# Kernel optimization log

Hardware: AMD Instinct MI355X
Metric: run time of the kernel (lower is better)

Reference implementation:

```python
import jax, jax.numpy as jnp
import numpy as np

BS, HW, HIDDEN, TOK, NTOK = 32, 1024, 256, 768, 2048


def setup_inputs() -> dict:
    key = jax.random.key(0)
    ks = jax.random.split(key, 6)
    s = 0.02  # init scale for weights
    return {
        "src": jax.random.normal(ks[0], (HW, BS, HIDDEN), jnp.float32),
        "codebook": jax.random.normal(ks[1], (NTOK, TOK), jnp.float32),
        "w_head": jax.random.normal(ks[2], (TOK, HIDDEN), jnp.float32) * s,
        "w_tail": jax.random.normal(ks[3], (HIDDEN, TOK), jnp.float32) * s,
        "w_pos": jax.random.normal(ks[4], (TOK, TOK), jnp.float32) * s,
        "b_pos": jnp.zeros((TOK,), jnp.float32),
        "w_gate": jax.random.normal(ks[5], (2, 2 * TOK), jnp.float32) * s,
        "h": 32,
        "w": 32,
    }


def reference(src, codebook, w_head, w_tail, w_pos, b_pos, w_gate, h, w):
    N, bs, hidden = src.shape  # [num_visu_token, bs, hidden_dim]
    tok = codebook.shape[1]
    # permute(1,2,0).view(bs,-1,h,w)
    x = jnp.transpose(src, (1, 2, 0)).reshape(bs, hidden, h, w)
    # conv_head: 1x1 conv, no bias
    xq = jnp.einsum("bchw,oc->bohw", x, w_head)  # [bs, tok, h, w]
    # raw-memory reshape, matches torch .view(-1, token_dim)
    flat = xq.reshape(-1, tok)  # [bs*h*w, tok]
    d = (
        jnp.sum(flat * flat, axis=1, keepdims=True)
        - 2.0 * flat @ codebook.T
        + jnp.sum(codebook * codebook, axis=1)[None, :]
    )
    indices = jnp.argmin(d, axis=1)  # [bs*h*w]
    quantized = codebook[indices]  # gather
    # straight-through estimator
    quantized = flat + jax.lax.stop_gradient(quantized - flat)
    # pos_align linear
    quantized = quantized @ w_pos.T + b_pos
    # view(bs, N, tok).permute(0,2,1).view(bs,-1,h,w)
    emb = jnp.transpose(quantized.reshape(bs, N, tok), (0, 2, 1)).reshape(bs, tok, h, w)
    # gated fusion
    gate_in = jnp.concatenate([emb, xq], axis=1)  # [bs, 2*tok, h, w]
    scores = jax.nn.softmax(jnp.einsum("bchw,oc->bohw", gate_in, w_gate), axis=1)
    fused = emb * scores[:, 0:1] + xq * scores[:, 1:2]
    # conv_tail 1x1, then flatten(2).permute(2,0,1)
    out = jnp.einsum("bchw,oc->bohw", fused, w_tail)  # [bs, hidden, h, w]
    out = jnp.transpose(out.reshape(bs, hidden, -1), (2, 0, 1))  # [h*w, bs, hidden]
    return out, indices
```

## Files before the change

kernel.cpp:

```cpp
#include <hip/hip_runtime.h>
#include <cstdint>

#define BSZ 32
#define NVIS 1024
#define HID 256
#define TOKD 768
#define NCODE 2048
#define NPIX 32768

typedef unsigned short u16;
typedef _Float16 half8 __attribute__((ext_vector_type(8)));
typedef unsigned short ushort8 __attribute__((ext_vector_type(8)));
typedef unsigned short u16x4 __attribute__((ext_vector_type(4)));
using f32x4 = __attribute__((ext_vector_type(4))) float;

#define AS1 __attribute__((address_space(1)))
#define AS3 __attribute__((address_space(3)))

__device__ __forceinline__ f32x4 mfmaF16(half8 a, half8 b, f32x4 c) {
  return __builtin_amdgcn_mfma_f32_16x16x32_f16(a, b, c, 0, 0, 0);
}

__device__ __forceinline__ unsigned long long pack_key(float d, int idx) {
  unsigned int b = __float_as_uint(d);
  b = (b & 0x80000000u) ? ~b : (b | 0x80000000u);
  return ((unsigned long long)b << 32) | (unsigned int)idx;
}

__device__ __forceinline__ void split16(float v, u16& h, u16& l) {
  union { _Float16 f; u16 u; } a, b;
  a.f = (_Float16)v;
  float hf = (float)a.f;
  b.f = (_Float16)(v - hf);
  h = a.u; l = b.u;
}

__global__ __launch_bounds__(256)
void prep1(const float* __restrict__ cb, const float* __restrict__ wh,
           const float* __restrict__ wt, const float* __restrict__ wp,
           const float* __restrict__ wg, const float* __restrict__ bp,
           u16* __restrict__ cbh, u16* __restrict__ cbl,
           u16* __restrict__ whh, u16* __restrict__ whl,
           float* __restrict__ cbn, float* __restrict__ Mm, float* __restrict__ uv,
           float* __restrict__ Gt, float* __restrict__ g2,
           float* __restrict__ ct0, float* __restrict__ cg) {
  const int bid = blockIdx.x, tid = threadIdx.x;
  if (bid < 6144) {
    int i = bid*256 + tid;
    u16 h, l; split16(cb[i], h, l);
    cbh[i] = h; cbl[i] = l;
  } else if (bid < 6912) {
    int i = (bid - 6144)*256 + tid;
    u16 h, l; split16(wh[i], h, l);
    whh[i] = h; whl[i] = l;
  } else if (bid < 7424) {
    int n = (bid - 6912)*4 + (tid >> 6);
    int lane = tid & 63;
    float a = 0.f;
#pragma unroll
    for (int i = 0; i < 12; ++i) { float v = cb[(long)n*TOKD + lane + 64*i]; a += v*v; }
#pragma unroll
    for (int off = 32; off; off >>= 1) a += __shfl_down(a, off);
    if (lane == 0) cbn[n] = a;
  } else if (bid < 7680) {
    int c2 = bid - 7424, c1 = tid;
    float acc = 0.f;
    for (int t = 0; t < TOKD; ++t) acc += wh[t*HID + c1] * wt[(long)c2*TOKD + t];
    Mm[c1*HID + c2] = acc;
  } else if (bid < 7682) {
    int o = bid - 7680, c1 = tid;
    float acc = 0.f;
    for (int t = 0; t < TOKD; ++t) acc += wh[t*HID + c1] * wg[o*(2*TOKD) + TOKD + t];
    uv[o*HID + c1] = acc;
  } else if (bid < 8450) {
    int rbid = bid - 7682;
    int c = rbid & 255, part = rbid >> 8;
    int tp = part*256 + tid;
    float acc = 0.f;
    for (int t = 0; t < TOKD; ++t) acc += wt[(long)c*TOKD + t] * wp[(long)t*TOKD + tp];
    Gt[(long)tp*HID + c] = acc;
  } else if (bid < 8453) {
    int tp = (bid - 8450)*256 + tid;
    float a0 = 0.f, a1 = 0.f;
    for (int t = 0; t < TOKD; ++t) {
      float wv = wp[(long)t*TOKD + tp];
      a0 += wv * wg[t];
      a1 += wv * wg[2*TOKD + t];
    }
    g2[tp] = a0; g2[TOKD + tp] = a1;
  } else if (bid < 8454) {
    int c = tid;
    float a = 0.f;
    for (int t = 0; t < TOKD; ++t) a += bp[t] * wt[(long)c*TOKD + t];
    ct0[c] = a;
  } else {
    int o = tid >> 6, lane = tid & 63;
    if (o < 2) {
      float a = 0.f;
      for (int t = lane; t < TOKD; t += 64) a += bp[t] * wg[o*(2*TOKD) + t];
#pragma unroll
      for (int off = 32; off; off >>= 1) a += __shfl_down(a, off);
      if (lane == 0) cg[o] = a;
    }
  }
}

__global__ __launch_bounds__(256)
void prep2(const float* __restrict__ cb, const float* __restrict__ Gt,
           const float* __restrict__ ct0, const float* __restrict__ g2,
           const float* __restrict__ cg, float* __restrict__ tc,
           float* __restrict__ gA) {
  __shared__ float cbs[8][TOKD];
  const int n0 = blockIdx.x * 8, tid = threadIdx.x;
  for (int i = tid; i < 8*TOKD; i += 256) cbs[i / TOKD][i % TOKD] = cb[(long)n0*TOKD + i];
  __syncthreads();
  float acc[8] = {};
  for (int t = 0; t < TOKD; ++t) {
    float gv = Gt[(long)t*HID + tid];
#pragma unroll
    for (int i = 0; i < 8; ++i) acc[i] += cbs[i][t] * gv;
  }
  float c0v = ct0[tid];
#pragma unroll
  for (int i = 0; i < 8; ++i) tc[(long)(n0+i)*HID + tid] = acc[i] + c0v;
  {
    int i = tid >> 5, l32 = tid & 31;
    float a0 = 0.f, a1 = 0.f;
    for (int t = l32; t < TOKD; t += 32) {
      float cv = cbs[i][t];
      a0 += cv * g2[t];
      a1 += cv * g2[TOKD + t];
    }
#pragma unroll
    for (int off = 16; off; off >>= 1) { a0 += __shfl_down(a0, off); a1 += __shfl_down(a1, off); }
    if (l32 == 0) { gA[n0+i] = a0 + cg[0]; gA[NCODE + n0+i] = a1 + cg[1]; }
  }
}

__global__ __launch_bounds__(256)
void head_mfma(const u16* __restrict__ whh, const u16* __restrict__ whl,
               const float* __restrict__ src,
               u16* __restrict__ xqh, u16* __restrict__ xql) {
  __shared__ u16 SM[32768] __attribute__((aligned(16)));
  u16* Ah = SM;
  u16* Al = SM + 8192;
  u16* Bh = SM + 16384;
  u16* Bl = SM + 24576;
  const int tid = threadIdx.x, lane = tid & 63, w = tid >> 6;
  const int n = lane & 15, q = lane >> 4;
  const int rh = w & 1, ch = w >> 1;
  const int obase = blockIdx.x * 128, pbase = blockIdx.y * 128, b = blockIdx.z;

  auto stageA = [&](int kc, int buf) {
#pragma unroll
    for (int is = 0; is < 2; ++is) {
      int c = is*256 + tid;
      int t = c >> 6, qq = (c >> 4) & 3, nn = c & 15;
      long off = (long)(obase + t*16 + nn)*HID + kc*32 + qq*8;
      __builtin_amdgcn_global_load_lds((AS1 void*)(whh + off),
          (AS3 void*)&Ah[buf*4096 + c*8], 16, 0, 0);
      __builtin_amdgcn_global_load_lds((AS1 void*)(whl + off),
          (AS3 void*)&Al[buf*4096 + c*8], 16, 0, 0);
    }
  };
  auto stageB = [&](int kc, int buf) {
#pragma unroll
    for (int is = 0; is < 4; ++is) {
      int x = is*256 + tid;
      int r = x >> 3;
      int d4 = (x & 7) * 4;
      const float* gp = src + ((long)(pbase + r)*BSZ + b)*HID + kc*32 + d4;
      float4 v = *(const float4*)gp;
      u16 h0,l0,h1,l1,h2,l2,h3,l3;
      split16(v.x, h0, l0); split16(v.y, h1, l1);
      split16(v.z, h2, l2); split16(v.w, h3, l3);
      int qq = d4 >> 3, j0 = (x & 1) * 4;
      int cc = (r >> 4)*64 + qq*16 + (r & 15);
      u16x4 hv = {h0, h1, h2, h3};
      u16x4 lv = {l0, l1, l2, l3};
      *(u16x4*)&Bh[buf*4096 + cc*8 + j0] = hv;
      *(u16x4*)&Bl[buf*4096 + cc*8 + j0] = lv;
    }
  };

  f32x4 acc[4][4];
#pragma unroll
  for (int i = 0; i < 4; ++i)
#pragma unroll
    for (int j = 0; j < 4; ++j) acc[i][j] = (f32x4){0.f, 0.f, 0.f, 0.f};

  stageA(0, 0); stageB(0, 0);
  __syncthreads();

  for (int kt = 0; kt < HID/32; ++kt) {
    const int buf = kt & 1;
    if (kt + 1 < HID/32) { stageA(kt + 1, buf ^ 1); stageB(kt + 1, buf ^ 1); }
    half8 af[4][2], bf[4][2];
#pragma unroll
    for (int rt = 0; rt < 4; ++rt) {
      int idx = buf*4096 + ((rh*4 + rt)*64 + q*16 + n)*8;
      af[rt][0] = *(const half8*)&Ah[idx];
      af[rt][1] = *(const half8*)&Al[idx];
    }
#pragma unroll
    for (int ct = 0; ct < 4; ++ct) {
      int idx = buf*4096 + ((ch*4 + ct)*64 + q*16 + n)*8;
      bf[ct][0] = *(const half8*)&Bh[idx];
      bf[ct][1] = *(const half8*)&Bl[idx];
    }
#pragma unroll
    for (int rt = 0; rt < 4; ++rt)
#pragma unroll
      for (int ct = 0; ct < 4; ++ct) {
        acc[rt][ct] = mfmaF16(af[rt][0], bf[ct][0], acc[rt][ct]);
        acc[rt][ct] = mfmaF16(af[rt][0], bf[ct][1], acc[rt][ct]);
        acc[rt][ct] = mfmaF16(af[rt][1], bf[ct][0], acc[rt][ct]);
      }
    __syncthreads();
  }

#pragma unroll
  for (int pass = 0; pass < 2; ++pass) {
    u16* dst = pass ? xql : xqh;
#pragma unroll
    for (int rt = 0; rt < 4; ++rt)
#pragma unroll
      for (int ct = 0; ct < 4; ++ct)
#pragma unroll
        for (int reg = 0; reg < 4; ++reg) {
          u16 hs, ls; split16(acc[rt][ct][reg], hs, ls);
          int ol = rh*64 + rt*16 + q*4 + reg;
          int pl = ch*64 + ct*16 + n;
          SM[ol*136 + pl] = pass ? ls : hs;
        }
    __syncthreads();
#pragma unroll
    for (int s = 0; s < 8; ++s) {
      int cc = tid*8 + s;
      int o = cc >> 4, p8 = cc & 15;
      ushort8 v = *(const ushort8*)&SM[o*136 + p8*8];
      long f = ((long)b*TOKD + obase + o)*NVIS + pbase + p8*8;
      long R = f / 768;
      int  C = (int)(f - R*768);
      long addr = (R >> 4)*12288 + (long)(C >> 5)*512
                + (long)((((C >> 3) & 3)*16 + (int)(R & 15))*8);
      *(ushort8*)(dst + addr) = v;
    }
    __syncthreads();
  }
}

__global__ __launch_bounds__(256)
void retile(u16* __restrict__ bufH, u16* __restrict__ bufL) {
  __shared__ u16 T[96*136] __attribute__((aligned(16)));
  const long tile = blockIdx.x;
  const int tid = threadIdx.x;
#pragma unroll
  for (int pass = 0; pass < 2; ++pass) {
    u16* buf = pass ? bufL : bufH;
    if (pass) __syncthreads();
#pragma unroll
    for (int i = 0; i < 6; ++i) {
      int g = i*256 + tid;
      int row = g / 96, c16 = g % 96;
      ushort8 v = *(const ushort8*)(buf + tile*12288 + row*768 + c16*8);
      *(ushort8*)&T[c16*136 + row*8] = v;
    }
    __syncthreads();
#pragma unroll
    for (int i = 0; i < 6; ++i) {
      int g = i*256 + tid;
      int kc = g >> 6, lp = g & 63;
      int q = lp >> 4, n = lp & 15;
      ushort8 v = *(const ushort8*)&T[(kc*4 + q)*136 + n*8];
      *(ushort8*)(buf + tile*12288 + (long)kc*512 + lp*8) = v;
    }
  }
}

__global__ __launch_bounds__(256, 2)
void vq_mfma(const u16* __restrict__ xqh, const u16* __restrict__ xql,
             const u16* __restrict__ cbh, const u16* __restrict__ cbl,
             const float* __restrict__ cbn, unsigned long long* __restrict__ keys) {
  const int bid = blockIdx.x;
  const int xcd = bid & 7, slot = bid >> 3;
  const int c2 = slot & 1, rowBlk = slot >> 1;
  const int codeBlkG = xcd * 2 + c2;
  const int rowTile0 = rowBlk * 16;
  const int codeTile0 = codeBlkG * 8;
  const int tid = threadIdx.x, lane = tid & 63, w = tid >> 6;
  const int n = lane & 15, q = lane >> 4;

  const u16* paH = xqh + (size_t)(rowTile0 + 4*w) * 12288 + lane*8;
  const u16* paL = xql + (size_t)(rowTile0 + 4*w) * 12288 + lane*8;
  const u16* pbH = cbh + (size_t)codeTile0 * 12288 + lane*8;
  const u16* pbL = cbl + (size_t)codeTile0 * 12288 + lane*8;

  auto LOAD_A = [&](int ht, half8 (&R)[4]) {
    const int sA = (ht >= 24 && ht < 48);
    const int kA = ht - ((ht >= 48) ? 48 : (sA ? 24 : 0));
    const u16* pa_ = (sA ? paL : paH) + kA*512;
#pragma unroll
    for (int i = 0; i < 4; ++i) R[i] = *(const half8*)(pa_ + (size_t)i*12288);
  };
  auto LOAD_B = [&](int ht, half8 (&R)[8]) {
    const int kB = ht - ((ht >= 48) ? 48 : ((ht >= 24) ? 24 : 0));
    const u16* pb_ = ((ht >= 48) ? pbL : pbH) + kB*512;
#pragma unroll
    for (int i = 0; i < 8; ++i) R[i] = *(const half8*)(pb_ + (size_t)i*12288);
  };

  f32x4 acc[4][8];
#pragma unroll
  for (int a = 0; a < 4; ++a)
#pragma unroll
    for (int b2 = 0; b2 < 8; ++b2) acc[a][b2] = (f32x4){0.f, 0.f, 0.f, 0.f};

  half8 Aa[4], Ab[4], Ba[8], Bb[8];

#define MFMA32(A_, B_)                                                       \
  {                                                                          \
    __builtin_amdgcn_s_setprio(1);                                           \
    _Pragma("unroll")                                                        \
    for (int rt = 0; rt < 4; ++rt)                                           \
      _Pragma("unroll")                                                      \
      for (int ct = 0; ct < 8; ++ct)                                         \
        acc[rt][ct] = mfmaF16(A_[rt], B_[ct], acc[rt][ct]);                  \
    __builtin_amdgcn_s_setprio(0);                                           \
  }

  LOAD_A(0, Aa); LOAD_B(0, Ba);
#pragma unroll 1
  for (int h2 = 0; h2 < 36; ++h2) {
    const int t0 = 2*h2;
    LOAD_A(t0 + 1, Ab); LOAD_B(t0 + 1, Bb);
    __builtin_amdgcn_sched_barrier(0);
    MFMA32(Aa, Ba);
    if (t0 + 2 < 72) { LOAD_A(t0 + 2, Aa); LOAD_B(t0 + 2, Ba); }
    __builtin_amdgcn_sched_barrier(0);
    MFMA32(Ab, Bb);
  }
#undef MFMA32

  float cbv[8];
#pragma unroll
  for (int ct = 0; ct < 8; ++ct) cbv[ct] = cbn[(codeTile0 + ct)*16 + n];
#pragma unroll
  for (int rt = 0; rt < 4; ++rt) {
#pragma unroll
    for (int reg = 0; reg < 4; ++reg) {
      float bd = 3.4e38f; int bi = 0;
#pragma unroll
      for (int ct = 0; ct < 8; ++ct) {
        float d = cbv[ct] - 2.0f * acc[rt][ct][reg];
        int code = (codeTile0 + ct)*16 + n;
        if (d < bd) { bd = d; bi = code; }
      }
      unsigned long long k = pack_key(bd, bi);
      unsigned long long v;
      v = __shfl_xor(k, 1); k = (v < k) ? v : k;
      v = __shfl_xor(k, 2); k = (v < k) ? v : k;
      v = __shfl_xor(k, 4); k = (v < k) ? v : k;
      v = __shfl_xor(k, 8); k = (v < k) ? v : k;
      if (n == 0) {
        int row = (rowTile0 + 4*w + rt)*16 + q*4 + reg;
        atomicMin(&keys[row], k);
      }
    }
  }
}

__global__ __launch_bounds__(256)
void fuse_out(const float* __restrict__ src, const unsigned long long* __restrict__ keys,
              const float* __restrict__ gA, const float* __restrict__ uvec,
              const float* __restrict__ Mm, const float* __restrict__ tailcode,
              float* __restrict__ out, float* __restrict__ outIdx) {
  __shared__ float ss[32][257];
  __shared__ float s0s[32];
  __shared__ int ids[32];
  const int tid = threadIdx.x;
  const int rb = blockIdx.x * 32;
  const int b = rb >> 10;
  const int p0 = rb & 1023;
#pragma unroll
  for (int qq = 0; qq < 32; ++qq)
    ss[qq][tid] = src[(long)(p0 + qq) * (BSZ*HID) + b*HID + tid];
  if (tid < 32) {
    unsigned long long u = keys[rb + tid];
    int id = (int)(unsigned int)(u & 0xFFFFFFFFull);
    ids[tid] = id;
    outIdx[rb + tid] = (float)id;
  }
  __syncthreads();
  {
    const int wv = tid >> 6, lane = tid & 63;
    for (int qq = 0; qq < 8; ++qq) {
      int qp = wv*8 + qq;
      float a0 = 0.f, a1 = 0.f;
#pragma unroll
      for (int i = 0; i < 4; ++i) {
        float v = ss[qp][lane + 64*i];
        a0 += v * uvec[lane + 64*i];
        a1 += v * uvec[HID + lane + 64*i];
      }
#pragma unroll
      for (int off = 32; off; off >>= 1) { a0 += __shfl_down(a0, off); a1 += __shfl_down(a1, off); }
      if (lane == 0) {
        int id = ids[qp];
        float l0 = gA[id] + a0;
        float l1 = gA[NCODE + id] + a1;
        s0s[qp] = 1.0f / (1.0f + expf(l1 - l0));
      }
    }
  }
  __syncthreads();
  const int qg = tid >> 5, cg = tid & 31;
  const int q0 = qg * 4, c0 = cg * 8;
  float acc[4][8] = {};
  for (int cp = 0; cp < HID; ++cp) {
    float4 m0 = *(const float4*)(Mm + cp*HID + c0);
    float4 m1 = *(const float4*)(Mm + cp*HID + c0 + 4);
    float mm[8] = {m0.x,m0.y,m0.z,m0.w,m1.x,m1.y,m1.z,m1.w};
#pragma unroll
    for (int i = 0; i < 4; ++i) {
      float sv = ss[q0+i][cp];
#pragma unroll
      for (int j = 0; j < 8; ++j) acc[i][j] += sv * mm[j];
    }
  }
#pragma unroll
  for (int i = 0; i < 4; ++i) {
    int qp = q0 + i;
    int id = ids[qp];
    float s0 = s0s[qp], s1 = 1.0f - s0;
    const float* tc = tailcode + (long)id*HID + c0;
    float* op = out + (long)(p0+qp)*(BSZ*HID) + b*HID + c0;
    float4 o0, o1;
    o0.x = s0*tc[0] + s1*acc[i][0]; o0.y = s0*tc[1] + s1*acc[i][1];
    o0.z = s0*tc[2] + s1*acc[i][2]; o0.w = s0*tc[3] + s1*acc[i][3];
    o1.x = s0*tc[4] + s1*acc[i][4]; o1.y = s0*tc[5] + s1*acc[i][5];
    o1.z = s0*tc[6] + s1*acc[i][6]; o1.w = s0*tc[7] + s1*acc[i][7];
    *(float4*)(op) = o0; *(float4*)(op+4) = o1;
  }
}

extern "C" void kernel_launch(void* const* d_in, const int* in_sizes, int n_in,
                              void* d_out, int out_size, void* d_ws, size_t ws_size,
                              hipStream_t stream) {
  const float* src    = (const float*)d_in[0];
  const float* cb     = (const float*)d_in[1];
  const float* w_head = (const float*)d_in[2];
  const float* w_tail = (const float*)d_in[3];
  const float* w_pos  = (const float*)d_in[4];
  const float* b_pos  = (const float*)d_in[5];
  const float* w_gate = (const float*)d_in[6];
  float* out = (float*)d_out;

  char* wsp = (char*)d_ws;
  size_t off = 0;
  auto alloc = [&](size_t bytes) {
    off = (off + 255) & ~(size_t)255;
    void* p = wsp + off; off += bytes; return p;
  };
  u16* xqh = (u16*)alloc((size_t)BSZ*TOKD*NVIS*2);
  u16* xql = (u16*)alloc((size_t)BSZ*TOKD*NVIS*2);
  u16* cbh = (u16*)alloc((size_t)NCODE*TOKD*2);
  u16* cbl = (u16*)alloc((size_t)NCODE*TOKD*2);
  u16* whh = (u16*)alloc((size_t)TOKD*HID*2);
  u16* whl = (u16*)alloc((size_t)TOKD*HID*2);
  float* cbn      = (float*)alloc((size_t)NCODE*4);
  float* Gt       = (float*)alloc((size_t)TOKD*HID*4);
  float* g2       = (float*)alloc((size_t)2*TOKD*4);
  float* ct0      = (float*)alloc((size_t)HID*4);
  float* cg       = (float*)alloc((size_t)2*4);
  float* tailcode = (float*)alloc((size_t)NCODE*HID*4);
  float* gA       = (float*)alloc((size_t)2*NCODE*4);
  float* Mm       = (float*)alloc((size_t)HID*HID*4);
  float* uvec     = (float*)alloc((size_t)2*HID*4);
  unsigned long long* keys = (unsigned long long*)alloc((size_t)NPIX*8);
  (void)ws_size; (void)in_sizes; (void)n_in; (void)out_size;

  prep1<<<8455, 256, 0, stream>>>(cb, w_head, w_tail, w_pos, w_gate, b_pos,
                                  cbh, cbl, whh, whl, cbn, Mm, uvec, Gt, g2, ct0, cg);
  retile<<<NCODE/16, 256, 0, stream>>>(cbh, cbl);
  prep2<<<NCODE/8, 256, 0, stream>>>(cb, Gt, ct0, g2, cg, tailcode, gA);

  head_mfma<<<dim3(TOKD/128, NVIS/128, BSZ), 256, 0, stream>>>(whh, whl, src, xqh, xql);

  hipMemsetAsync(keys, 0xFF, (size_t)NPIX*8, stream);
  vq_mfma<<<2048, 256, 0, stream>>>(xqh, xql, cbh, cbl, cbn, keys);

  fuse_out<<<NPIX/32, 256, 0, stream>>>(src, keys, gA, uvec, Mm, tailcode,
                                        out, out + (size_t)NVIS*BSZ*HID);
}
```

Baseline: 700.7 us.

## Stage codebook tiles in LDS via async global_load_lds and remap block grid

The VQ distance MFMA kernel now stages the codebook (B) hi/lo fragments into a 4-slot LDS ring with global_load_lds, shared by all four waves, instead of each wave loading all 8 B tiles straight from global memory. The K loop is restructured to 24 steps, each doing the three split-precision products (AH·BH, AL·BH, AH·BL) with A still read from global. Block-to-XCD mapping changes so each XCD owns contiguous row blocks and iterates all code blocks. The aim is to cut redundant global and L2 traffic for the codebook. The cost is a barrier per step and manual vmcnt waits that must match the prefetch depth.

Result: faster. 659.3 us (-5.9%).

```diff
diff --git a/kernel.cpp b/kernel.cpp
--- a/kernel.cpp
+++ b/kernel.cpp
@@ -282,33 +282,32 @@
 void vq_mfma(const u16* __restrict__ xqh, const u16* __restrict__ xql,
              const u16* __restrict__ cbh, const u16* __restrict__ cbl,
              const float* __restrict__ cbn, unsigned long long* __restrict__ keys) {
+  __shared__ u16 SM[32768] __attribute__((aligned(16)));
   const int bid = blockIdx.x;
   const int xcd = bid & 7, slot = bid >> 3;
-  const int c2 = slot & 1, rowBlk = slot >> 1;
-  const int codeBlkG = xcd * 2 + c2;
+  const int rowBlk = xcd * 16 + (slot >> 4);
+  const int codeBlk = slot & 15;
   const int rowTile0 = rowBlk * 16;
-  const int codeTile0 = codeBlkG * 8;
+  const int codeTile0 = codeBlk * 8;
   const int tid = threadIdx.x, lane = tid & 63, w = tid >> 6;
   const int n = lane & 15, q = lane >> 4;
 
   const u16* paH = xqh + (size_t)(rowTile0 + 4*w) * 12288 + lane*8;
   const u16* paL = xql + (size_t)(rowTile0 + 4*w) * 12288 + lane*8;
-  const u16* pbH = cbh + (size_t)codeTile0 * 12288 + lane*8;
-  const u16* pbL = cbl + (size_t)codeTile0 * 12288 + lane*8;
-
-  auto LOAD_A = [&](int ht, half8 (&R)[4]) {
-    const int sA = (ht >= 24 && ht < 48);
-    const int kA = ht - ((ht >= 48) ? 48 : (sA ? 24 : 0));
-    const u16* pa_ = (sA ? paL : paH) + kA*512;
-#pragma unroll
-    for (int i = 0; i < 4; ++i) R[i] = *(const half8*)(pa_ + (size_t)i*12288);
+  const u16* pbH0 = cbh + (size_t)(codeTile0 + 2*w) * 12288 + lane*8;
+  const u16* pbL0 = cbl + (size_t)(codeTile0 + 2*w) * 12288 + lane*8;
+  const int bChunk = (2*w)*512 + lane*8;
+
+  auto STAGE_B = [&](int kk, int buf) {
+    const u16* ph = pbH0 + kk*512;
+    const u16* pl = pbL0 + kk*512;
+    u16* lh_ = &SM[buf*8192 + bChunk];
+    u16* ll_ = &SM[buf*8192 + 4096 + bChunk];
+    __builtin_amdgcn_global_load_lds((AS1 void*)ph,           (AS3 void*)lh_,         16, 0, 0);
+    __builtin_amdgcn_global_load_lds((AS1 void*)(ph + 12288), (AS3 void*)(lh_ + 512), 16, 0, 0);
+    __builtin_amdgcn_global_load_lds((AS1 void*)pl,           (AS3 void*)ll_,         16, 0, 0);
+    __builtin_amdgcn_global_load_lds((AS1 void*)(pl + 12288), (AS3 void*)(ll_ + 512), 16, 0, 0);
   };
-  auto LOAD_B = [&](int ht, half8 (&R)[8]) {
-    const int kB = ht - ((ht >= 48) ? 48 : ((ht >= 24) ? 24 : 0));
-    const u16* pb_ = ((ht >= 48) ? pbL : pbH) + kB*512;
-#pragma unroll
-    for (int i = 0; i < 8; ++i) R[i] = *(const half8*)(pb_ + (size_t)i*12288);
-  };
 
   f32x4 acc[4][8];
 #pragma unroll
@@ -316,31 +315,47 @@
 #pragma unroll
     for (int b2 = 0; b2 < 8; ++b2) acc[a][b2] = (f32x4){0.f, 0.f, 0.f, 0.f};
 
-  half8 Aa[4], Ab[4], Ba[8], Bb[8];
-
-#define MFMA32(A_, B_)                                                       \
-  {                                                                          \
-    __builtin_amdgcn_s_setprio(1);                                           \
-    _Pragma("unroll")                                                        \
-    for (int rt = 0; rt < 4; ++rt)                                           \
-      _Pragma("unroll")                                                      \
-      for (int ct = 0; ct < 8; ++ct)                                         \
-        acc[rt][ct] = mfmaF16(A_[rt], B_[ct], acc[rt][ct]);                  \
-    __builtin_amdgcn_s_setprio(0);                                           \
-  }
-
-  LOAD_A(0, Aa); LOAD_B(0, Ba);
+  half8 AH[4], AL[4], Bf[8];
+
+  STAGE_B(0, 0); STAGE_B(1, 1);
+  asm volatile("s_waitcnt vmcnt(0)" ::: "memory");
+  asm volatile("s_barrier" ::: "memory");
+
 #pragma unroll 1
-  for (int h2 = 0; h2 < 36; ++h2) {
-    const int t0 = 2*h2;
-    LOAD_A(t0 + 1, Ab); LOAD_B(t0 + 1, Bb);
-    __builtin_amdgcn_sched_barrier(0);
-    MFMA32(Aa, Ba);
-    if (t0 + 2 < 72) { LOAD_A(t0 + 2, Aa); LOAD_B(t0 + 2, Ba); }
-    __builtin_amdgcn_sched_barrier(0);
-    MFMA32(Ab, Bb);
-  }
-#undef MFMA32
+  for (int kk = 0; kk < 24; ++kk) {
+    const int pf = (kk + 2 > 23) ? 23 : kk + 2;
+    STAGE_B(pf, (kk + 2) & 3);
+#pragma unroll
+    for (int i = 0; i < 4; ++i) AH[i] = *(const half8*)(paH + kk*512 + (size_t)i*12288);
+#pragma unroll
+    for (int i = 0; i < 4; ++i) AL[i] = *(const half8*)(paL + kk*512 + (size_t)i*12288);
+    const int bb = (kk & 3)*8192;
+#pragma unroll
+    for (int ct = 0; ct < 8; ++ct) Bf[ct] = *(const half8*)&SM[bb + ct*512 + lane*8];
+    __builtin_amdgcn_s_setprio(1);
+#pragma unroll
+    for (int rt = 0; rt < 4; ++rt)
+#pragma unroll
+      for (int ct = 0; ct < 8; ++ct)
+        acc[rt][ct] = mfmaF16(AH[rt], Bf[ct], acc[rt][ct]);
+#pragma unroll
+    for (int rt = 0; rt < 4; ++rt)
+#pragma unroll
+      for (int ct = 0; ct < 8; ++ct)
+        acc[rt][ct] = mfmaF16(AL[rt], Bf[ct], acc[rt][ct]);
+    __builtin_amdgcn_s_setprio(0);
+#pragma unroll
+    for (int ct = 0; ct < 8; ++ct) Bf[ct] = *(const half8*)&SM[bb + 4096 + ct*512 + lane*8];
+    __builtin_amdgcn_s_setprio(1);
+#pragma unroll
+    for (int rt = 0; rt < 4; ++rt)
+#pragma unroll
+      for (int ct = 0; ct < 8; ++ct)
+        acc[rt][ct] = mfmaF16(AH[rt], Bf[ct], acc[rt][ct]);
+    __builtin_amdgcn_s_setprio(0);
+    asm volatile("s_waitcnt vmcnt(12)" ::: "memory");
+    asm volatile("s_barrier" ::: "memory");
+  }
 
   float cbv[8];
 #pragma unroll
```
